# Performance work log

Measured on AMD Instinct MI355X. Metric: run time of the kernel, lower is better.

## Reference

```python
import jax, jax.numpy as jnp
import numpy as np

EPS = 1e-06
N, K, O = 100000, 64, 1024


def setup_inputs() -> dict:
    key = jax.random.key(0)
    k1, k2, k3 = jax.random.split(key, 3)
    # counts: non-negative read counts per particle (scaled uniform, like count data)
    counts = jnp.floor(jax.random.uniform(k1, (N, O), dtype=jnp.float32) * 10.0)
    # otu_dist: K community profiles over O OTUs (simplex rows)
    otu_raw = jax.random.uniform(k2, (K, O), dtype=jnp.float32) + 1e-3
    otu_dist = otu_raw / otu_raw.sum(axis=-1, keepdims=True)
    # comm_dist: mixture weights over K communities (simplex)
    comm_raw = jax.random.uniform(k3, (K,), dtype=jnp.float32) + 1e-3
    comm_dist = comm_raw / comm_raw.sum()
    return {"counts": counts, "otu_dist": otu_dist, "comm_dist": comm_dist}


def reference(counts, otu_dist, comm_dist):
    # (counts[:,None,:] * log(otu_dist[None,:,:]+EPS)).sum(-1) == counts @ log(otu_dist+EPS).T
    # (N,K) per-particle per-community log-likelihood + log prior weight
    log_otu = jnp.log(otu_dist + EPS)                      # (K, O)
    logsumexpand = jnp.einsum('no,ko->nk', counts, log_otu) + jnp.log(comm_dist + EPS)[None, :]
    summand = jax.scipy.special.logsumexp(logsumexpand, axis=1)  # (N,)
    return summand.sum()
```

## Files before the change

### kernel.cpp

```cpp
#include <hip/hip_runtime.h>
#include <hip/hip_bf16.h>
#include <math.h>

#define NP 100000
#define KC 64
#define OD 1024
#define EPSF 1e-6f

#define ROWS_PER_BLOCK 128
#define NBLOCKS ((NP + ROWS_PER_BLOCK - 1) / ROWS_PER_BLOCK)
#define NT 16

typedef __attribute__((ext_vector_type(8))) short short8;
typedef __attribute__((ext_vector_type(4))) float f32x4;

#define WS_LOGW      0
#define WS_PARTIALS  256
#define WS_BSTAGE    8192

__device__ __forceinline__ unsigned short f32_bf16_rn(float f) {
  unsigned int u = __float_as_uint(f);
  unsigned int r = u + 0x7fffu + ((u >> 16) & 1u);
  return (unsigned short)(r >> 16);
}

__device__ __forceinline__ void gll16(const void* gsrc, void* lds) {
  __builtin_amdgcn_global_load_lds(
      (const __attribute__((address_space(1))) unsigned int*)gsrc,
      (__attribute__((address_space(3))) unsigned int*)lds, 16, 0, 0);
}

__global__ void prep_kernel(const float* __restrict__ otu,
                            const float* __restrict__ comm,
                            unsigned short* __restrict__ bstage,
                            float* __restrict__ logw) {
  int b = blockIdx.x;
  if (b < KC) {
    int c = b & 15, ct = b >> 4;
    for (int k = threadIdx.x; k < OD; k += blockDim.x) {
      float x = logf(otu[b * OD + k] + EPSF);
      unsigned short h = f32_bf16_rn(x);
      float hf = __uint_as_float(((unsigned int)h) << 16);
      unsigned short l = f32_bf16_rn(x - hf);
      int t = k >> 6, kg = (k >> 5) & 1, g = (k >> 3) & 3, kk = k & 7;
      size_t base = (size_t)t * 8192 + (size_t)kg * 2048 + (size_t)ct * 512
                  + (size_t)(g * 16 + c) * 8 + kk;
      bstage[base] = h;
      bstage[base + 4096] = l;
    }
  } else {
    if (threadIdx.x < KC) logw[threadIdx.x] = logf(comm[threadIdx.x] + EPSF);
  }
}

__global__ __launch_bounds__(256, 3)
void ll_kernel(const float* __restrict__ counts,
               const unsigned short* __restrict__ bstage,
               const float* __restrict__ logw,
               double* __restrict__ partials) {
  __shared__ unsigned short bufB[2][8192];

  const int tid = threadIdx.x;
  const int wave = tid >> 6;
  const int lane = tid & 63;
  const int g = lane >> 4;
  const int c = lane & 15;
  const int rowBase = blockIdx.x * ROWS_PER_BLOCK + wave * 32;

  f32x4 acc[2][4];
#pragma unroll
  for (int i = 0; i < 2; ++i)
#pragma unroll
    for (int j = 0; j < 4; ++j)
      acc[i][j] = (f32x4){0.f, 0.f, 0.f, 0.f};

  int r0 = rowBase + c;      if (r0 >= NP) r0 = NP - 1;
  int r1 = rowBase + 16 + c; if (r1 >= NP) r1 = NP - 1;
  const float* pa0 = counts + (size_t)r0 * OD + g * 8;
  const float* pa1 = counts + (size_t)r1 * OD + g * 8;

  const unsigned short* sbase = bstage + (size_t)wave * 2048 + (size_t)lane * 8;

  {
    unsigned short* dst = &bufB[0][wave * 2048];
    gll16(sbase, dst);
    gll16(sbase + 512, dst + 512);
    gll16(sbase + 1024, dst + 1024);
    gll16(sbase + 1536, dst + 1536);
  }
  __syncthreads();

  int cur = 0;
  for (int t = 0; t < NT; ++t) {
    const int tn = (t + 1 < NT) ? t + 1 : NT - 1;

    {
      const unsigned short* src = sbase + (size_t)tn * 8192;
      unsigned short* dst = &bufB[cur ^ 1][wave * 2048];
      gll16(src, dst);
      gll16(src + 512, dst + 512);
      gll16(src + 1024, dst + 1024);
      gll16(src + 1536, dst + 1536);
    }

    const float* a0p = pa0 + t * 64;
    const float* a1p = pa1 + t * 64;
    float4 A0[2][2], A1[2][2];
#pragma unroll
    for (int kg = 0; kg < 2; ++kg) {
      A0[kg][0] = *(const float4*)(a0p + kg * 32);
      A0[kg][1] = *(const float4*)(a0p + kg * 32 + 4);
      A1[kg][0] = *(const float4*)(a1p + kg * 32);
      A1[kg][1] = *(const float4*)(a1p + kg * 32 + 4);
    }

#pragma unroll
    for (int kg = 0; kg < 2; ++kg) {
      short8 fbh[4], fbl[4];
#pragma unroll
      for (int ct = 0; ct < 4; ++ct) {
        fbh[ct] = *(const short8*)(&bufB[cur][kg * 2048 + ct * 512 + lane * 8]);
        fbl[ct] = *(const short8*)(&bufB[cur][4096 + kg * 2048 + ct * 512 + lane * 8]);
      }

      union { unsigned int u[4]; short8 v; } ua0, ua1;
      ua0.u[0] = __builtin_amdgcn_perm(__float_as_uint(A0[kg][0].y), __float_as_uint(A0[kg][0].x), 0x07060302u);
      ua0.u[1] = __builtin_amdgcn_perm(__float_as_uint(A0[kg][0].w), __float_as_uint(A0[kg][0].z), 0x07060302u);
      ua0.u[2] = __builtin_amdgcn_perm(__float_as_uint(A0[kg][1].y), __float_as_uint(A0[kg][1].x), 0x07060302u);
      ua0.u[3] = __builtin_amdgcn_perm(__float_as_uint(A0[kg][1].w), __float_as_uint(A0[kg][1].z), 0x07060302u);
      ua1.u[0] = __builtin_amdgcn_perm(__float_as_uint(A1[kg][0].y), __float_as_uint(A1[kg][0].x), 0x07060302u);
      ua1.u[1] = __builtin_amdgcn_perm(__float_as_uint(A1[kg][0].w), __float_as_uint(A1[kg][0].z), 0x07060302u);
      ua1.u[2] = __builtin_amdgcn_perm(__float_as_uint(A1[kg][1].y), __float_as_uint(A1[kg][1].x), 0x07060302u);
      ua1.u[3] = __builtin_amdgcn_perm(__float_as_uint(A1[kg][1].w), __float_as_uint(A1[kg][1].z), 0x07060302u);

#pragma unroll
      for (int ct = 0; ct < 4; ++ct) {
        acc[0][ct] = __builtin_amdgcn_mfma_f32_16x16x32_bf16(ua0.v, fbh[ct], acc[0][ct], 0, 0, 0);
        acc[1][ct] = __builtin_amdgcn_mfma_f32_16x16x32_bf16(ua1.v, fbh[ct], acc[1][ct], 0, 0, 0);
        acc[0][ct] = __builtin_amdgcn_mfma_f32_16x16x32_bf16(ua0.v, fbl[ct], acc[0][ct], 0, 0, 0);
        acc[1][ct] = __builtin_amdgcn_mfma_f32_16x16x32_bf16(ua1.v, fbl[ct], acc[1][ct], 0, 0, 0);
      }
    }

    __syncthreads();
    cur ^= 1;
  }

  float lw[4];
#pragma unroll
  for (int ct = 0; ct < 4; ++ct) lw[ct] = logw[ct * 16 + c];

  double lsum = 0.0;
#pragma unroll
  for (int rt = 0; rt < 2; ++rt) {
#pragma unroll
    for (int r = 0; r < 4; ++r) {
      float v0 = acc[rt][0][r] + lw[0];
      float v1 = acc[rt][1][r] + lw[1];
      float v2 = acc[rt][2][r] + lw[2];
      float v3 = acc[rt][3][r] + lw[3];
      float m = fmaxf(fmaxf(v0, v1), fmaxf(v2, v3));
      m = fmaxf(m, __shfl_xor(m, 1));
      m = fmaxf(m, __shfl_xor(m, 2));
      m = fmaxf(m, __shfl_xor(m, 4));
      m = fmaxf(m, __shfl_xor(m, 8));
      float s = __expf(v0 - m) + __expf(v1 - m) + __expf(v2 - m) + __expf(v3 - m);
      s += __shfl_xor(s, 1);
      s += __shfl_xor(s, 2);
      s += __shfl_xor(s, 4);
      s += __shfl_xor(s, 8);
      float lse = m + __logf(s);
      int row = rowBase + rt * 16 + g * 4 + r;
      if (c == 0 && row < NP) lsum += (double)lse;
    }
  }
  lsum += __shfl_xor(lsum, 16);
  lsum += __shfl_xor(lsum, 32);

  __shared__ double wpart[4];
  if (lane == 0) wpart[wave] = lsum;
  __syncthreads();
  if (tid == 0) partials[blockIdx.x] = wpart[0] + wpart[1] + wpart[2] + wpart[3];
}

__global__ void finalize_kernel(const double* __restrict__ partials,
                                float* __restrict__ out) {
  double s = 0.0;
  for (int i = threadIdx.x; i < NBLOCKS; i += 256) s += partials[i];
  s += __shfl_xor(s, 1);
  s += __shfl_xor(s, 2);
  s += __shfl_xor(s, 4);
  s += __shfl_xor(s, 8);
  s += __shfl_xor(s, 16);
  s += __shfl_xor(s, 32);
  __shared__ double sp[4];
  int w = threadIdx.x >> 6, lane = threadIdx.x & 63;
  if (lane == 0) sp[w] = s;
  __syncthreads();
  if (threadIdx.x == 0) out[0] = (float)(sp[0] + sp[1] + sp[2] + sp[3]);
}

extern "C" void kernel_launch(void* const* d_in, const int* in_sizes, int n_in,
                              void* d_out, int out_size, void* d_ws, size_t ws_size,
                              hipStream_t stream) {
  const float* counts = (const float*)d_in[0];
  const float* otu    = (const float*)d_in[1];
  const float* comm   = (const float*)d_in[2];
  float* out = (float*)d_out;
  char* ws = (char*)d_ws;

  float* logw          = (float*)(ws + WS_LOGW);
  double* partials     = (double*)(ws + WS_PARTIALS);
  unsigned short* bst  = (unsigned short*)(ws + WS_BSTAGE);

  prep_kernel<<<KC + 1, 256, 0, stream>>>(otu, comm, bst, logw);
  ll_kernel<<<NBLOCKS, 256, 0, stream>>>(counts, bst, logw, partials);
  finalize_kernel<<<1, 256, 0, stream>>>(partials, out);
}
```

Measured before the change: 585.1 us.

## Read B fragments directly from global and batch count loads per quarter

Drops the LDS double buffer and per-tile barriers for the bf16 log-profile operand. Each lane now reads its B fragments directly from global memory, which should hit in L2 or L1. The K loop is restructured into four chunks of 256 columns with all count loads for a chunk issued up front, raising memory-level parallelism. The starting chunk is rotated by block index to spread access. Occupancy is lowered to two blocks per CU to hold the larger register set, at the cost of fewer waves hiding latency and repeated global B reads.

Result: faster. 564.1 us (-3.6%).

```diff
diff --git a/kernel.cpp b/kernel.cpp
--- a/kernel.cpp
+++ b/kernel.cpp
@@ -9,7 +9,6 @@
 
 #define ROWS_PER_BLOCK 128
 #define NBLOCKS ((NP + ROWS_PER_BLOCK - 1) / ROWS_PER_BLOCK)
-#define NT 16
 
 typedef __attribute__((ext_vector_type(8))) short short8;
 typedef __attribute__((ext_vector_type(4))) float f32x4;
@@ -24,12 +23,6 @@
   return (unsigned short)(r >> 16);
 }
 
-__device__ __forceinline__ void gll16(const void* gsrc, void* lds) {
-  __builtin_amdgcn_global_load_lds(
-      (const __attribute__((address_space(1))) unsigned int*)gsrc,
-      (__attribute__((address_space(3))) unsigned int*)lds, 16, 0, 0);
-}
-
 __global__ void prep_kernel(const float* __restrict__ otu,
                             const float* __restrict__ comm,
                             unsigned short* __restrict__ bstage,
@@ -42,24 +35,22 @@
       unsigned short h = f32_bf16_rn(x);
       float hf = __uint_as_float(((unsigned int)h) << 16);
       unsigned short l = f32_bf16_rn(x - hf);
-      int t = k >> 6, kg = (k >> 5) & 1, g = (k >> 3) & 3, kk = k & 7;
-      size_t base = (size_t)t * 8192 + (size_t)kg * 2048 + (size_t)ct * 512
+      int kb = k >> 5, g = (k >> 3) & 3, kk = k & 7;
+      size_t base = (size_t)kb * 4096 + (size_t)ct * 512
                   + (size_t)(g * 16 + c) * 8 + kk;
       bstage[base] = h;
-      bstage[base + 4096] = l;
+      bstage[base + 2048] = l;
     }
   } else {
     if (threadIdx.x < KC) logw[threadIdx.x] = logf(comm[threadIdx.x] + EPSF);
   }
 }
 
-__global__ __launch_bounds__(256, 3)
+__global__ __launch_bounds__(256, 2)
 void ll_kernel(const float* __restrict__ counts,
                const unsigned short* __restrict__ bstage,
                const float* __restrict__ logw,
                double* __restrict__ partials) {
-  __shared__ unsigned short bufB[2][8192];
-
   const int tid = threadIdx.x;
   const int wave = tid >> 6;
   const int lane = tid & 63;
@@ -79,71 +70,56 @@
   const float* pa0 = counts + (size_t)r0 * OD + g * 8;
   const float* pa1 = counts + (size_t)r1 * OD + g * 8;
 
-  const unsigned short* sbase = bstage + (size_t)wave * 2048 + (size_t)lane * 8;
+  const int p = blockIdx.x & 3;
 
-  {
-    unsigned short* dst = &bufB[0][wave * 2048];
-    gll16(sbase, dst);
-    gll16(sbase + 512, dst + 512);
-    gll16(sbase + 1024, dst + 1024);
-    gll16(sbase + 1536, dst + 1536);
-  }
-  __syncthreads();
+  for (int ci = 0; ci < 4; ++ci) {
+    const int t = (p + ci) & 3;
+    const float* a0 = pa0 + t * 256;
+    const float* a1 = pa1 + t * 256;
 
-  int cur = 0;
-  for (int t = 0; t < NT; ++t) {
-    const int tn = (t + 1 < NT) ? t + 1 : NT - 1;
-
-    {
-      const unsigned short* src = sbase + (size_t)tn * 8192;
-      unsigned short* dst = &bufB[cur ^ 1][wave * 2048];
-      gll16(src, dst);
-      gll16(src + 512, dst + 512);
-      gll16(src + 1024, dst + 1024);
-      gll16(src + 1536, dst + 1536);
+    float4 x0[8], x1[8], y0[8], y1[8];
+#pragma unroll
+    for (int s = 0; s < 8; ++s) {
+      x0[s] = *(const float4*)(a0 + s * 32);
+      x1[s] = *(const float4*)(a0 + s * 32 + 4);
+      y0[s] = *(const float4*)(a1 + s * 32);
+      y1[s] = *(const float4*)(a1 + s * 32 + 4);
     }
 
-    const float* a0p = pa0 + t * 64;
-    const float* a1p = pa1 + t * 64;
-    float4 A0[2][2], A1[2][2];
+    short8 ah0[8], ah1[8];
 #pragma unroll
-    for (int kg = 0; kg < 2; ++kg) {
-      A0[kg][0] = *(const float4*)(a0p + kg * 32);
-      A0[kg][1] = *(const float4*)(a0p + kg * 32 + 4);
-      A1[kg][0] = *(const float4*)(a1p + kg * 32);
-      A1[kg][1] = *(const float4*)(a1p + kg * 32 + 4);
+    for (int s = 0; s < 8; ++s) {
+      union { unsigned int u[4]; short8 v; } u0, u1;
+      u0.u[0] = __builtin_amdgcn_perm(__float_as_uint(x0[s].y), __float_as_uint(x0[s].x), 0x07060302u);
+      u0.u[1] = __builtin_amdgcn_perm(__float_as_uint(x0[s].w), __float_as_uint(x0[s].z), 0x07060302u);
+      u0.u[2] = __builtin_amdgcn_perm(__float_as_uint(x1[s].y), __float_as_uint(x1[s].x), 0x07060302u);
+      u0.u[3] = __builtin_amdgcn_perm(__float_as_uint(x1[s].w), __float_as_uint(x1[s].z), 0x07060302u);
+      u1.u[0] = __builtin_amdgcn_perm(__float_as_uint(y0[s].y), __float_as_uint(y0[s].x), 0x07060302u);
+      u1.u[1] = __builtin_amdgcn_perm(__float_as_uint(y0[s].w), __float_as_uint(y0[s].z), 0x07060302u);
+      u1.u[2] = __builtin_amdgcn_perm(__float_as_uint(y1[s].y), __float_as_uint(y1[s].x), 0x07060302u);
+      u1.u[3] = __builtin_amdgcn_perm(__float_as_uint(y1[s].w), __float_as_uint(y1[s].z), 0x07060302u);
+      ah0[s] = u0.v;
+      ah1[s] = u1.v;
     }
 
 #pragma unroll
-    for (int kg = 0; kg < 2; ++kg) {
+    for (int s = 0; s < 8; ++s) {
+      const int kb = t * 8 + s;
+      const unsigned short* bb = bstage + (size_t)kb * 4096 + (size_t)lane * 8;
       short8 fbh[4], fbl[4];
 #pragma unroll
       for (int ct = 0; ct < 4; ++ct) {
-        fbh[ct] = *(const short8*)(&bufB[cur][kg * 2048 + ct * 512 + lane * 8]);
-        fbl[ct] = *(const short8*)(&bufB[cur][4096 + kg * 2048 + ct * 512 + lane * 8]);
+        fbh[ct] = *(const short8*)(bb + ct * 512);
+        fbl[ct] = *(const short8*)(bb + 2048 + ct * 512);
       }
-
-      union { unsigned int u[4]; short8 v; } ua0, ua1;
-      ua0.u[0] = __builtin_amdgcn_perm(__float_as_uint(A0[kg][0].y), __float_as_uint(A0[kg][0].x), 0x07060302u);
-      ua0.u[1] = __builtin_amdgcn_perm(__float_as_uint(A0[kg][0].w), __float_as_uint(A0[kg][0].z), 0x07060302u);
-      ua0.u[2] = __builtin_amdgcn_perm(__float_as_uint(A0[kg][1].y), __float_as_uint(A0[kg][1].x), 0x07060302u);
-      ua0.u[3] = __builtin_amdgcn_perm(__float_as_uint(A0[kg][1].w), __float_as_uint(A0[kg][1].z), 0x07060302u);
-      ua1.u[0] = __builtin_amdgcn_perm(__float_as_uint(A1[kg][0].y), __float_as_uint(A1[kg][0].x), 0x07060302u);
-      ua1.u[1] = __builtin_amdgcn_perm(__float_as_uint(A1[kg][0].w), __float_as_uint(A1[kg][0].z), 0x07060302u);
-      ua1.u[2] = __builtin_amdgcn_perm(__float_as_uint(A1[kg][1].y), __float_as_uint(A1[kg][1].x), 0x07060302u);
-      ua1.u[3] = __builtin_amdgcn_perm(__float_as_uint(A1[kg][1].w), __float_as_uint(A1[kg][1].z), 0x07060302u);
-
 #pragma unroll
       for (int ct = 0; ct < 4; ++ct) {
-        acc[0][ct] = __builtin_amdgcn_mfma_f32_16x16x32_bf16(ua0.v, fbh[ct], acc[0][ct], 0, 0, 0);
-        acc[1][ct] = __builtin_amdgcn_mfma_f32_16x16x32_bf16(ua1.v, fbh[ct], acc[1][ct], 0, 0, 0);
-        acc[0][ct] = __builtin_amdgcn_mfma_f32_16x16x32_bf16(ua0.v, fbl[ct], acc[0][ct], 0, 0, 0);
-        acc[1][ct] = __builtin_amdgcn_mfma_f32_16x16x32_bf16(ua1.v, fbl[ct], acc[1][ct], 0, 0, 0);
+        acc[0][ct] = __builtin_amdgcn_mfma_f32_16x16x32_bf16(ah0[s], fbh[ct], acc[0][ct], 0, 0, 0);
+        acc[1][ct] = __builtin_amdgcn_mfma_f32_16x16x32_bf16(ah1[s], fbh[ct], acc[1][ct], 0, 0, 0);
+        acc[0][ct] = __builtin_amdgcn_mfma_f32_16x16x32_bf16(ah0[s], fbl[ct], acc[0][ct], 0, 0, 0);
+        acc[1][ct] = __builtin_amdgcn_mfma_f32_16x16x32_bf16(ah1[s], fbl[ct], acc[1][ct], 0, 0, 0);
       }
     }
-
-    __syncthreads();
-    cur ^= 1;
   }
 
   float lw[4];
```
